# Performance work log

Hardware: AMD Instinct MI355X
Metric: run time of the kernel (lower is better)

Reference implementation:

```python
import jax, jax.numpy as jnp
import numpy as np

D_MODEL = 1024
N_HEADS = 16
D_HEAD = D_MODEL // N_HEADS
D_FF = 4096
EPS = 1e-5


def _layernorm(x, g, b):
    mu = jnp.mean(x, axis=-1, keepdims=True)
    var = jnp.mean(jnp.square(x - mu), axis=-1, keepdims=True)
    return (x - mu) * jax.lax.rsqrt(var + EPS) * g + b


def setup_inputs() -> dict:
    key = jax.random.key(0)
    ks = jax.random.split(key, 16)
    B, S, D = 2, 2048, D_MODEL

    def xavier(k, shape):
        fan_in, fan_out = shape[0], shape[1]
        lim = float(np.sqrt(6.0 / (fan_in + fan_out)))
        return jax.random.uniform(k, shape, jnp.float32, -lim, lim)

    return {
        "x": jax.random.normal(ks[0], (B, S, D), jnp.float32),
        "ln1_g": jnp.ones((D,), jnp.float32),
        "ln1_b": jnp.zeros((D,), jnp.float32),
        "wq": xavier(ks[1], (D, D)), "bq": jnp.zeros((D,), jnp.float32),
        "wk": xavier(ks[2], (D, D)), "bk": jnp.zeros((D,), jnp.float32),
        "wv": xavier(ks[3], (D, D)), "bv": jnp.zeros((D,), jnp.float32),
        "wo": xavier(ks[4], (D, D)), "bo": jnp.zeros((D,), jnp.float32),
        "wf": xavier(ks[5], (D, N_HEADS)), "bf": jnp.zeros((N_HEADS,), jnp.float32),
        "ln2_g": jnp.ones((D,), jnp.float32),
        "ln2_b": jnp.zeros((D,), jnp.float32),
        "w1": xavier(ks[6], (D, D_FF)), "b1": jnp.zeros((D_FF,), jnp.float32),
        "w2": xavier(ks[7], (D_FF, D)), "b2": jnp.zeros((D,), jnp.float32),
    }


def reference(x, ln1_g, ln1_b, wq, bq, wk, bk, wv, bv, wo, bo, wf, bf,
              ln2_g, ln2_b, w1, b1, w2, b2):
    B, S, D = x.shape
    H, Dh = N_HEADS, D_HEAD

    # --- pre-norm forgetting attention ---
    h = _layernorm(x, ln1_g, ln1_b)
    q = (h @ wq + bq).reshape(B, S, H, Dh)
    k = (h @ wk + bk).reshape(B, S, H, Dh)
    v = (h @ wv + bv).reshape(B, S, H, Dh)

    # per-head scalar forget gate f_t in (0,1); cumulative log-decay c_t
    logf = jax.nn.log_sigmoid(h @ wf + bf)           # (B, S, H)
    c = jnp.cumsum(logf, axis=1)                     # (B, S, H)

    scale = 1.0 / jnp.sqrt(jnp.asarray(Dh, x.dtype))
    logits = jnp.einsum("bihd,bjhd->bhij", q, k) * scale
    # decay bias D_ij = c_i - c_j (sum of log forget gates in (j, i])
    decay = c.transpose(0, 2, 1)                     # (B, H, S)
    logits = logits + decay[:, :, :, None] - decay[:, :, None, :]

    causal = jnp.tril(jnp.ones((S, S), bool))
    logits = jnp.where(causal[None, None], logits, -jnp.inf)

    attn = jax.nn.softmax(logits, axis=-1)           # (B, H, S, S)
    ctx = jnp.einsum("bhij,bjhd->bihd", attn, v).reshape(B, S, D)
    attn_out = ctx @ wo + bo

    x = x + attn_out                                 # dropout = identity (eval)

    # --- pre-norm GELU MLP ---
    h2 = _layernorm(x, ln2_g, ln2_b)
    ff = jax.nn.gelu(h2 @ w1 + b1, approximate=False) @ w2 + b2
    return x + ff
```

## Files before the change

kernel.cpp:

```cpp
#include <hip/hip_runtime.h>
#include <hip/hip_bf16.h>
#include <math.h>

typedef unsigned short u16;
typedef unsigned int u32;
typedef __bf16 bf16x8 __attribute__((ext_vector_type(8)));
typedef float f32x4 __attribute__((ext_vector_type(4)));
typedef u32 u32x4 __attribute__((ext_vector_type(4)));

__device__ __forceinline__ u16 f2bf(float f) {
  __hip_bfloat16 h = __float2bfloat16(f);
  return *reinterpret_cast<u16*>(&h);
}
__device__ __forceinline__ float bf2f(u16 u) {
  return __uint_as_float(((u32)u) << 16);
}

#define GLL(gp, lp)                                                     \
  __builtin_amdgcn_global_load_lds(                                     \
      (const __attribute__((address_space(1))) void*)(gp),              \
      (__attribute__((address_space(3))) void*)(lp), 16, 0, 0)

__global__ __launch_bounds__(256) void transpose_cast(
    const float* __restrict__ in, u16* __restrict__ out, int R, int C) {
  __shared__ float tile[32][33];
  int c0 = blockIdx.x * 32, r0 = blockIdx.y * 32;
  int tx = threadIdx.x & 31, ty = threadIdx.x >> 5;
  for (int i = ty; i < 32; i += 8) {
    int r = r0 + i, c = c0 + tx;
    if (r < R && c < C) tile[i][tx] = in[(size_t)r * C + c];
  }
  __syncthreads();
  for (int i = ty; i < 32; i += 8) {
    int c = c0 + i, r = r0 + tx;
    if (c < C && r < R) out[(size_t)c * R + r] = f2bf(tile[tx][i]);
  }
}

__global__ __launch_bounds__(256) void transpose_cast3(
    const float* __restrict__ in0, const float* __restrict__ in1,
    const float* __restrict__ in2, u16* __restrict__ out) {
  __shared__ float tile[32][33];
  const float* in = (blockIdx.z == 0) ? in0 : (blockIdx.z == 1) ? in1 : in2;
  u16* o = out + (size_t)blockIdx.z * 1024 * 1024;
  int c0 = blockIdx.x * 32, r0 = blockIdx.y * 32;
  int tx = threadIdx.x & 31, ty = threadIdx.x >> 5;
  for (int i = ty; i < 32; i += 8)
    tile[i][tx] = in[(size_t)(r0 + i) * 1024 + c0 + tx];
  __syncthreads();
  for (int i = ty; i < 32; i += 8)
    o[(size_t)(c0 + i) * 1024 + r0 + tx] = f2bf(tile[tx][i]);
}

__global__ __launch_bounds__(256) void pack3(
    const float* __restrict__ a, const float* __restrict__ b,
    const float* __restrict__ c, float* __restrict__ o, u32* __restrict__ ctr) {
  int t = blockIdx.x * 256 + threadIdx.x;
  if (t == 0) *ctr = 0u;
  if (t < 1024) o[t] = a[t];
  else if (t < 2048) o[t] = b[t - 1024];
  else if (t < 3072) o[t] = c[t - 2048];
}

__global__ __launch_bounds__(256) void ln_kernel(
    const float* x, const float* __restrict__ g,
    const float* __restrict__ bb, u16* __restrict__ out,
    float* xadd, const float* addb) {
  __shared__ float red[8];
  const int row = blockIdx.x;
  const float* xr = x + (size_t)row * 1024;
  f32x4 v = *(const f32x4*)(xr + threadIdx.x * 4);
  float s = v[0] + v[1] + v[2] + v[3];
  #pragma unroll
  for (int off = 32; off > 0; off >>= 1) s += __shfl_xor(s, off, 64);
  if ((threadIdx.x & 63) == 0) red[threadIdx.x >> 6] = s;
  __syncthreads();
  float mu = (red[0] + red[1] + red[2] + red[3]) * (1.0f / 1024.0f);
  f32x4 d;
  d[0] = v[0] - mu; d[1] = v[1] - mu; d[2] = v[2] - mu; d[3] = v[3] - mu;
  float sq = d[0]*d[0] + d[1]*d[1] + d[2]*d[2] + d[3]*d[3];
  #pragma unroll
  for (int off = 32; off > 0; off >>= 1) sq += __shfl_xor(sq, off, 64);
  if ((threadIdx.x & 63) == 0) red[4 + (threadIdx.x >> 6)] = sq;
  __syncthreads();
  float var = (red[4] + red[5] + red[6] + red[7]) * (1.0f / 1024.0f);
  float rstd = rsqrtf(var + 1e-5f);
  int cb = threadIdx.x * 4;
  #pragma unroll
  for (int e = 0; e < 4; ++e)
    out[(size_t)row * 1024 + cb + e] = f2bf(d[e] * rstd * g[cb + e] + bb[cb + e]);
  if (xadd) {
    f32x4 w;
    #pragma unroll
    for (int e = 0; e < 4; ++e) w[e] = v[e] + addb[cb + e];
    *(f32x4*)(xadd + (size_t)row * 1024 + cb) = w;
  }
}

__global__ __launch_bounds__(256) void gemm_bt(
    const u16* __restrict__ A, const u16* __restrict__ Bt,
    const float* __restrict__ bias, const float* __restrict__ res,
    void* __restrict__ outp, int M, int N, int K, int mode) {
  __shared__ u16 As[4 * 128 * 32];
  __shared__ u16 Bs[4 * 128 * 32];
  const int tid = threadIdx.x;
  const int m0 = blockIdx.y * 128, n0 = blockIdx.x * 128;
  const int wave = tid >> 6, lane = tid & 63;
  const int wm = (wave >> 1) * 64, wn = (wave & 1) * 64;
  const int lr = lane & 15, quad = lane >> 4;
  const int g0 = wave * 2;
  const int srow0 = g0 * 16 + (lane >> 2);
  const int scol = (lane & 3) * 8;
  const u16* Ag0 = A + (size_t)(m0 + srow0) * K + scol;
  const u16* Ag1 = A + (size_t)(m0 + srow0 + 16) * K + scol;
  const u16* Bg0 = Bt + (size_t)(n0 + srow0) * K + scol;
  const u16* Bg1 = Bt + (size_t)(n0 + srow0 + 16) * K + scol;
  const int ao0 = g0 * 512, ao1 = (g0 + 1) * 512;

  f32x4 acc[4][4] = {};

  GLL(Ag0, As + ao0); GLL(Ag1, As + ao1);
  GLL(Bg0, Bs + ao0); GLL(Bg1, Bs + ao1);
  if (K > 32) {
    GLL(Ag0 + 32, As + 4096 + ao0); GLL(Ag1 + 32, As + 4096 + ao1);
    GLL(Bg0 + 32, Bs + 4096 + ao0); GLL(Bg1 + 32, Bs + 4096 + ao1);
  }

  for (int k0 = 0; k0 < K; k0 += 32) {
    const int cb = ((k0 >> 5) & 3) * 4096;
    if (k0 + 64 < K) {
      const int pb = (((k0 >> 5) + 2) & 3) * 4096;
      GLL(Ag0 + k0 + 64, As + pb + ao0);
      GLL(Ag1 + k0 + 64, As + pb + ao1);
      GLL(Bg0 + k0 + 64, Bs + pb + ao0);
      GLL(Bg1 + k0 + 64, Bs + pb + ao1);
      asm volatile("s_waitcnt vmcnt(8)" ::: "memory");
    } else if (k0 + 32 < K) {
      asm volatile("s_waitcnt vmcnt(4)" ::: "memory");
    } else {
      asm volatile("s_waitcnt vmcnt(0)" ::: "memory");
    }
    __builtin_amdgcn_s_barrier();
    __builtin_amdgcn_sched_barrier(0);
    bf16x8 af[4], bfr[4];
    #pragma unroll
    for (int t = 0; t < 4; ++t) {
      af[t]  = *(const bf16x8*)&As[cb + (wm + t * 16 + lr) * 32 + quad * 8];
      bfr[t] = *(const bf16x8*)&Bs[cb + (wn + t * 16 + lr) * 32 + quad * 8];
    }
    #pragma unroll
    for (int mt = 0; mt < 4; ++mt)
      #pragma unroll
      for (int nt = 0; nt < 4; ++nt)
        acc[mt][nt] = __builtin_amdgcn_mfma_f32_16x16x32_bf16(
            af[mt], bfr[nt], acc[mt][nt], 0, 0, 0);
  }

  #pragma unroll
  for (int mt = 0; mt < 4; ++mt) {
    #pragma unroll
    for (int nt = 0; nt < 4; ++nt) {
      const int col = n0 + wn + nt * 16 + lr;
      const float bvv = bias[col];
      #pragma unroll
      for (int rr = 0; rr < 4; ++rr) {
        const int row = m0 + wm + mt * 16 + quad * 4 + rr;
        const size_t idx = (size_t)row * N + col;
        float v = acc[mt][nt][rr] + bvv;
        if (mode == 0) {
          ((float*)outp)[idx] = v;
        } else if (mode == 1) {
          ((float*)outp)[idx] = v + res[idx];
        } else if (mode == 2) {
          float gl = 0.5f * v * (1.0f + erff(v * 0.70710678118654752f));
          ((u16*)outp)[idx] = f2bf(gl);
        } else {
          ((u16*)outp)[idx] = f2bf(v);
        }
      }
    }
  }
}

__global__ __launch_bounds__(256) void gemm_bt_sk(
    const u16* __restrict__ A, const u16* __restrict__ Bt,
    float* __restrict__ outp, int M, int N, int Ktot, int Kslice) {
  __shared__ u16 As[4 * 128 * 32];
  __shared__ u16 Bs[4 * 128 * 32];
  const int tid = threadIdx.x;
  const int m0 = blockIdx.y * 128, n0 = blockIdx.x * 128;
  const int kbeg = blockIdx.z * Kslice, kend = kbeg + Kslice;
  const int wave = tid >> 6, lane = tid & 63;
  const int wm = (wave >> 1) * 64, wn = (wave & 1) * 64;
  const int lr = lane & 15, quad = lane >> 4;
  const int g0 = wave * 2;
  const int srow0 = g0 * 16 + (lane >> 2);
  const int scol = (lane & 3) * 8;
  const u16* Ag0 = A + (size_t)(m0 + srow0) * Ktot + scol;
  const u16* Ag1 = A + (size_t)(m0 + srow0 + 16) * Ktot + scol;
  const u16* Bg0 = Bt + (size_t)(n0 + srow0) * Ktot + scol;
  const u16* Bg1 = Bt + (size_t)(n0 + srow0 + 16) * Ktot + scol;
  const int ao0 = g0 * 512, ao1 = (g0 + 1) * 512;

  f32x4 acc[4][4] = {};

  GLL(Ag0 + kbeg, As + ao0); GLL(Ag1 + kbeg, As + ao1);
  GLL(Bg0 + kbeg, Bs + ao0); GLL(Bg1 + kbeg, Bs + ao1);
  if (kbeg + 32 < kend) {
    GLL(Ag0 + kbeg + 32, As + 4096 + ao0); GLL(Ag1 + kbeg + 32, As + 4096 + ao1);
    GLL(Bg0 + kbeg + 32, Bs + 4096 + ao0); GLL(Bg1 + kbeg + 32, Bs + 4096 + ao1);
  }

  for (int k0 = kbeg; k0 < kend; k0 += 32) {
    const int st = (k0 - kbeg) >> 5;
    const int cb = (st & 3) * 4096;
    if (k0 + 64 < kend) {
      const int pb = ((st + 2) & 3) * 4096;
      GLL(Ag0 + k0 + 64, As + pb + ao0);
      GLL(Ag1 + k0 + 64, As + pb + ao1);
      GLL(Bg0 + k0 + 64, Bs + pb + ao0);
      GLL(Bg1 + k0 + 64, Bs + pb + ao1);
      asm volatile("s_waitcnt vmcnt(8)" ::: "memory");
    } else if (k0 + 32 < kend) {
      asm volatile("s_waitcnt vmcnt(4)" ::: "memory");
    } else {
      asm volatile("s_waitcnt vmcnt(0)" ::: "memory");
    }
    __builtin_amdgcn_s_barrier();
    __builtin_amdgcn_sched_barrier(0);
    bf16x8 af[4], bfr[4];
    #pragma unroll
    for (int t = 0; t < 4; ++t) {
      af[t]  = *(const bf16x8*)&As[cb + (wm + t * 16 + lr) * 32 + quad * 8];
      bfr[t] = *(const bf16x8*)&Bs[cb + (wn + t * 16 + lr) * 32 + quad * 8];
    }
    #pragma unroll
    for (int mt = 0; mt < 4; ++mt)
      #pragma unroll
      for (int nt = 0; nt < 4; ++nt)
        acc[mt][nt] = __builtin_amdgcn_mfma_f32_16x16x32_bf16(
            af[mt], bfr[nt], acc[mt][nt], 0, 0, 0);
  }

  #pragma unroll
  for (int mt = 0; mt < 4; ++mt) {
    #pragma unroll
    for (int nt = 0; nt < 4; ++nt) {
      const int col = n0 + wn + nt * 16 + lr;
      #pragma unroll
      for (int rr = 0; rr < 4; ++rr) {
        const int row = m0 + wm + mt * 16 + quad * 4 + rr;
        __hip_atomic_fetch_add(&outp[(size_t)row * N + col], acc[mt][nt][rr],
                               __ATOMIC_RELAXED, __HIP_MEMORY_SCOPE_AGENT);
      }
    }
  }
}

__global__ __launch_bounds__(256) void gemm_n64(
    const u16* __restrict__ A, const u16* __restrict__ Bt,
    const float* __restrict__ bias, const float* __restrict__ res,
    void* __restrict__ outp, int M, int N, int K, int mode) {
  __shared__ u16 As[4 * 128 * 32];
  __shared__ u16 Bs[4 * 64 * 32];
  const int tid = threadIdx.x;
  const int m0 = blockIdx.y * 128, n0 = blockIdx.x * 64;
  const int wave = tid >> 6, lane = tid & 63;
  const int wm = (wave >> 1) * 64, wn = (wave & 1) * 32;
  const int lr = lane & 15, quad = lane >> 4;
  const int g0 = wave * 2;
  const int srow = lane >> 2;
  const int scol = (lane & 3) * 8;
  const u16* Ag0 = A + (size_t)(m0 + g0 * 16 + srow) * K + scol;
  const u16* Ag1 = A + (size_t)(m0 + g0 * 16 + 16 + srow) * K + scol;
  const u16* Bg  = Bt + (size_t)(n0 + wave * 16 + srow) * K + scol;
  const int ao0 = g0 * 512, ao1 = (g0 + 1) * 512, bo = wave * 512;

  f32x4 acc[4][2] = {};

  GLL(Ag0, As + ao0); GLL(Ag1, As + ao1); GLL(Bg, Bs + bo);
  if (K > 32) {
    GLL(Ag0 + 32, As + 4096 + ao0); GLL(Ag1 + 32, As + 4096 + ao1);
    GLL(Bg + 32, Bs + 2048 + bo);
  }

  for (int k0 = 0; k0 < K; k0 += 32) {
    const int st = k0 >> 5;
    const int cba = (st & 3) * 4096, cbb = (st & 3) * 2048;
    if (k0 + 64 < K) {
      const int pba = ((st + 2) & 3) * 4096, pbb = ((st + 2) & 3) * 2048;
      GLL(Ag0 + k0 + 64, As + pba + ao0);
      GLL(Ag1 + k0 + 64, As + pba + ao1);
      GLL(Bg + k0 + 64, Bs + pbb + bo);
      asm volatile("s_waitcnt vmcnt(6)" ::: "memory");
    } else if (k0 + 32 < K) {
      asm volatile("s_waitcnt vmcnt(3)" ::: "memory");
    } else {
      asm volatile("s_waitcnt vmcnt(0)" ::: "memory");
    }
    __builtin_amdgcn_s_barrier();
    __builtin_amdgcn_sched_barrier(0);
    bf16x8 af[4], bfr[2];
    #pragma unroll
    for (int t = 0; t < 4; ++t)
      af[t] = *(const bf16x8*)&As[cba + (wm + t * 16 + lr) * 32 + quad * 8];
    #pragma unroll
    for (int t = 0; t < 2; ++t)
      bfr[t] = *(const bf16x8*)&Bs[cbb + (wn + t * 16 + lr) * 32 + quad * 8];
    #pragma unroll
    for (int mt = 0; mt < 4; ++mt)
      #pragma unroll
      for (int nt = 0; nt < 2; ++nt)
        acc[mt][nt] = __builtin_amdgcn_mfma_f32_16x16x32_bf16(
            af[mt], bfr[nt], acc[mt][nt], 0, 0, 0);
  }

  #pragma unroll
  for (int mt = 0; mt < 4; ++mt) {
    #pragma unroll
    for (int nt = 0; nt < 2; ++nt) {
      const int col = n0 + wn + nt * 16 + lr;
      const float bvv = bias[col];
      #pragma unroll
      for (int rr = 0; rr < 4; ++rr) {
        const int row = m0 + wm + mt * 16 + quad * 4 + rr;
        const size_t idx = (size_t)row * N + col;
        float v = acc[mt][nt][rr] + bvv;
        if (mode == 0) {
          ((float*)outp)[idx] = v;
        } else if (mode == 1) {
          ((float*)outp)[idx] = v + res[idx];
        } else if (mode == 2) {
          float gl = 0.5f * v * (1.0f + erff(v * 0.70710678118654752f));
          ((u16*)outp)[idx] = f2bf(gl);
        } else {
          ((u16*)outp)[idx] = f2bf(v);
        }
      }
    }
  }
}

__global__ __launch_bounds__(64) void logf_kernel(
    const u16* __restrict__ h, const u16* __restrict__ wfT,
    const float* __restrict__ bfv, float* __restrict__ c) {
  const int row = blockIdx.x;
  const int lane = threadIdx.x;
  float acc[16];
  #pragma unroll
  for (int n = 0; n < 16; ++n) acc[n] = 0.f;
  for (int t = 0; t < 16; ++t) {
    int kidx = t * 64 + lane;
    float hv = bf2f(h[(size_t)row * 1024 + kidx]);
    #pragma unroll
    for (int n = 0; n < 16; ++n)
      acc[n] += hv * bf2f(wfT[n * 1024 + kidx]);
  }
  float z = 0.f;
  #pragma unroll
  for (int n = 0; n < 16; ++n) {
    float r = acc[n];
    #pragma unroll
    for (int off = 1; off < 64; off <<= 1) r += __shfl_xor(r, off, 64);
    if (lane == n) z = r;
  }
  if (lane < 16) {
    z += bfv[lane];
    float lf = (z >= 0.f) ? -log1pf(expf(-z)) : (z - log1pf(expf(z)));
    c[(size_t)row * 16 + lane] = lf;
  }
}

__global__ __launch_bounds__(64) void cumsum_kernel(float* __restrict__ c, int S) {
  const int b = blockIdx.x >> 4, h = blockIdx.x & 15;
  const int lane = threadIdx.x;
  float carry = 0.f;
  for (int s0 = 0; s0 < S; s0 += 64) {
    float v = c[(size_t)(b * S + s0 + lane) * 16 + h];
    #pragma unroll
    for (int off = 1; off < 64; off <<= 1) {
      float t = __shfl_up(v, off, 64);
      if (lane >= off) v += t;
    }
    v += carry;
    c[(size_t)(b * S + s0 + lane) * 16 + h] = v;
    carry = __shfl(v, 63, 64);
  }
}

__global__ __launch_bounds__(256) void vtrans(
    const u16* __restrict__ qkvb, u16* __restrict__ vtg) {
  __shared__ u16 t[32][33];
  const int bh = blockIdx.z, b = bh >> 4, h = bh & 15;
  const int s0 = blockIdx.x * 32, d0 = blockIdx.y * 32;
  const int tx = threadIdx.x & 31, ty = threadIdx.x >> 5;
  for (int i = ty; i < 32; i += 8)
    t[i][tx] = qkvb[(size_t)(b * 2048 + s0 + i) * 3072 + 2048 + h * 64 + d0 + tx];
  __syncthreads();
  for (int i = ty; i < 32; i += 8)
    vtg[(size_t)(bh * 64 + d0 + i) * 2048 + s0 + tx] = t[tx][i];
}

__global__ __launch_bounds__(64) void qk_norms(
    const u16* __restrict__ qkvb, float* __restrict__ qkmax) {
  const int tile = blockIdx.x, bh = blockIdx.y, z = blockIdx.z;
  const int b = bh >> 4, h = bh & 15;
  const int tok = tile * 64 + (int)threadIdx.x;
  const u16* p = qkvb + (size_t)(b * 2048 + tok) * 3072 + z * 1024 + h * 64;
  float s = 0.f;
  #pragma unroll
  for (int i = 0; i < 4; ++i) {
    u32x4 w = *(const u32x4*)(p + i * 16);
    u32x4 w2 = *(const u32x4*)(p + i * 16 + 8);
    #pragma unroll
    for (int e = 0; e < 4; ++e) {
      float lo = __uint_as_float(w[e] << 16);
      float hi = __uint_as_float(w[e] & 0xffff0000u);
      float lo2 = __uint_as_float(w2[e] << 16);
      float hi2 = __uint_as_float(w2[e] & 0xffff0000u);
      s += lo * lo + hi * hi + lo2 * lo2 + hi2 * hi2;
    }
  }
  s = sqrtf(s);
  #pragma unroll
  for (int off = 1; off < 64; off <<= 1) s = fmaxf(s, __shfl_xor(s, off, 64));
  if (threadIdx.x == 0) qkmax[z * 1024 + bh * 32 + tile] = s;
}

#define FS 72
#define NITEMS 1024
#define L2E 1.4426950408889634f

__global__ __launch_bounds__(256) void fattn(
    const u16* __restrict__ qkvb, const u16* __restrict__ vtg,
    const float* __restrict__ c, const float* __restrict__ qkmax,
    u16* __restrict__ ctx, u32* __restrict__ ctr) {
  __shared__ u16 Qs[64 * FS];
  __shared__ u16 Ks[64 * FS];
  __shared__ u16 Vt[64 * FS];
  __shared__ u16 Ps[64 * FS];
  __shared__ float cjs[64];
  __shared__ float wmn[4];
  __shared__ u32 sh_item;
  const int S = 2048;
  const int tid = threadIdx.x, wave = tid >> 6, lane = tid & 63;
  const int lr = lane & 15, quad = lane >> 4;
  const int w16 = wave * 16;
  const int sr = tid >> 2, scc = (tid & 3) * 16;

  for (;;) {
    if (tid == 0) sh_item = atomicAdd(ctr, 1u);
    __syncthreads();
    const u32 item = sh_item;
    if (item >= NITEMS) return;
    const int qt = 31 - (int)(item >> 5);
    const int bh = (int)(item & 31), b = bh >> 4, h = bh & 15;
    const int i0 = qt * 64;

    {
      const u16* src = qkvb + (size_t)(b * S + i0 + sr) * 3072 + h * 64 + scc;
      *(u32x4*)&Qs[sr * FS + scc] = *(const u32x4*)src;
      *(u32x4*)&Qs[sr * FS + scc + 8] = *(const u32x4*)(src + 8);
    }
    u32x4 kr0, kr1, vr0, vr1;
    float cjr = 0.f;
    {
      const u16* ks = qkvb + (size_t)(b * S + i0 + sr) * 3072 + 1024 + h * 64 + scc;
      kr0 = *(const u32x4*)ks;
      kr1 = *(const u32x4*)(ks + 8);
      const u16* vs = vtg + (size_t)(bh * 64 + sr) * 2048 + i0 + scc;
      vr0 = *(const u32x4*)vs;
      vr1 = *(const u32x4*)(vs + 8);
      if (tid < 64) cjr = c[(size_t)(b * S + i0 + tid) * 16 + h];
    }
    float bscale;
    {
      float qm = qkmax[bh * 32 + qt];
      float km = 0.f;
      for (int t = 0; t <= qt; ++t) km = fmaxf(km, qkmax[1024 + bh * 32 + t]);
      bscale = qm * km * (0.125f * L2E);
    }
    float m_[4], l_[4], alpha[4];
    f32x4 o_[4];
    #pragma unroll
    for (int r = 0; r < 4; ++r) {
      m_[r] = -INFINITY;
      l_[r] = 0.f;
    }
    #pragma unroll
    for (int dt = 0; dt < 4; ++dt) o_[dt] = (f32x4){0.f, 0.f, 0.f, 0.f};

    __syncthreads();
    const bf16x8 aq0 = *(const bf16x8*)&Qs[(w16 + lr) * FS + quad * 8];
    const bf16x8 aq1 = *(const bf16x8*)&Qs[(w16 + lr) * FS + 32 + quad * 8];

    for (int jt = qt; jt >= 0; --jt) {
      const int j0 = jt * 64;
      *(u32x4*)&Ks[sr * FS + scc] = kr0;
      *(u32x4*)&Ks[sr * FS + scc + 8] = kr1;
      *(u32x4*)&Vt[sr * FS + scc] = vr0;
      *(u32x4*)&Vt[sr * FS + scc + 8] = vr1;
      if (tid < 64) cjs[tid] = cjr * L2E;
      if (jt > 0) {
        const int j1 = j0 - 64;
        const u16* ks = qkvb + (size_t)(b * S + j1 + sr) * 3072 + 1024 + h * 64 + scc;
        kr0 = *(const u32x4*)ks;
        kr1 = *(const u32x4*)(ks + 8);
        const u16* vs = vtg + (size_t)(bh * 64 + sr) * 2048 + j1 + scc;
        vr0 = *(const u32x4*)vs;
        vr1 = *(const u32x4*)(vs + 8);
        if (tid < 64) cjr = c[(size_t)(b * S + j1 + tid) * 16 + h];
      }
      __syncthreads();

      f32x4 sc[4];
      #pragma unroll
      for (int nt = 0; nt < 4; ++nt) {
        bf16x8 bk0 = *(const bf16x8*)&Ks[(nt * 16 + lr) * FS + quad * 8];
        bf16x8 bk1 = *(const bf16x8*)&Ks[(nt * 16 + lr) * FS + 32 + quad * 8];
        f32x4 z = {0.f, 0.f, 0.f, 0.f};
        z = __builtin_amdgcn_mfma_f32_16x16x32_bf16(aq0, bk0, z, 0, 0, 0);
        z = __builtin_amdgcn_mfma_f32_16x16x32_bf16(aq1, bk1, z, 0, 0, 0);
        sc[nt] = z;
      }
      const bool diag = (jt == qt);
      #pragma unroll
      for (int r = 0; r < 4; ++r) {
        const int i = i0 + w16 + quad * 4 + r;
        float lg[4], mrow = -INFINITY;
        #pragma unroll
        for (int nt = 0; nt < 4; ++nt) {
          const int j = j0 + nt * 16 + lr;
          float v = sc[nt][r] * (0.125f * L2E) - cjs[nt * 16 + lr];
          if (diag && (j > i)) v = -INFINITY;
          lg[nt] = v;
          mrow = fmaxf(mrow, v);
        }
        #pragma unroll
        for (int off = 1; off < 16; off <<= 1)
          mrow = fmaxf(mrow, __shfl_xor(mrow, off, 64));
        const float mn = fmaxf(m_[r], mrow);
        alpha[r] = __builtin_exp2f(m_[r] - mn);
        m_[r] = mn;
        float rs = 0.f;
        #pragma unroll
        for (int nt = 0; nt < 4; ++nt) {
          const float p = __builtin_exp2f(lg[nt] - mn);
          Ps[(w16 + quad * 4 + r) * FS + nt * 16 + lr] = f2bf(p);
          rs += p;
        }
        l_[r] = l_[r] * alpha[r] + rs;
      }
      asm volatile("s_waitcnt lgkmcnt(0)" ::: "memory");
      #pragma unroll
      for (int dt = 0; dt < 4; ++dt)
        #pragma unroll
        for (int r = 0; r < 4; ++r) o_[dt][r] *= alpha[r];
      bf16x8 ap0 = *(const bf16x8*)&Ps[(w16 + lr) * FS + quad * 8];
      bf16x8 ap1 = *(const bf16x8*)&Ps[(w16 + lr) * FS + 32 + quad * 8];
      #pragma unroll
      for (int dt = 0; dt < 4; ++dt) {
        bf16x8 bv0 = *(const bf16x8*)&Vt[(dt * 16 + lr) * FS + quad * 8];
        bf16x8 bv1 = *(const bf16x8*)&Vt[(dt * 16 + lr) * FS + 32 + quad * 8];
        o_[dt] = __builtin_amdgcn_mfma_f32_16x16x32_bf16(ap0, bv0, o_[dt], 0, 0, 0);
        o_[dt] = __builtin_amdgcn_mfma_f32_16x16x32_bf16(ap1, bv1, o_[dt], 0, 0, 0);
      }
      {
        float wmin = fminf(fminf(m_[0], m_[1]), fminf(m_[2], m_[3]));
        wmin = fminf(wmin, __shfl_xor(wmin, 16, 64));
        wmin = fminf(wmin, __shfl_xor(wmin, 32, 64));
        if (lane == 0) wmn[wave] = wmin;
      }
      __syncthreads();
      if (jt > 0) {
        const float bmin = fminf(fminf(wmn[0], wmn[1]), fminf(wmn[2], wmn[3]));
        const float cend = c[(size_t)(b * S + j0 - 1) * 16 + h];
        if (bscale - cend * L2E < bmin - 40.f) break;
      }
    }
    #pragma unroll
    for (int r = 0; r < 4; ++r) {
      float lt = l_[r];
      #pragma unroll
      for (int off = 1; off < 16; off <<= 1) lt += __shfl_xor(lt, off, 64);
      const float inv = 1.0f / lt;
      const size_t base = (size_t)(b * S + i0 + w16 + quad * 4 + r) * 1024 + h * 64;
      #pragma unroll
      for (int dt = 0; dt < 4; ++dt)
        ctx[base + dt * 16 + lr] = f2bf(o_[dt][r] * inv);
    }
  }
}

extern "C" void kernel_launch(void* const* d_in, const int* in_sizes, int n_in,
                              void* d_out, int out_size, void* d_ws, size_t ws_size,
                              hipStream_t stream) {
  const float* x    = (const float*)d_in[0];
  const float* ln1g = (const float*)d_in[1];
  const float* ln1b = (const float*)d_in[2];
  const float* wq   = (const float*)d_in[3];
  const float* bq   = (const float*)d_in[4];
  const float* wk   = (const float*)d_in[5];
  const float* bk   = (const float*)d_in[6];
  const float* wv   = (const float*)d_in[7];
  const float* bv   = (const float*)d_in[8];
  const float* wo   = (const float*)d_in[9];
  const float* bo   = (const float*)d_in[10];
  const float* wf   = (const float*)d_in[11];
  const float* bfv  = (const float*)d_in[12];
  const float* ln2g = (const float*)d_in[13];
  const float* ln2b = (const float*)d_in[14];
  const float* w1   = (const float*)d_in[15];
  const float* b1   = (const float*)d_in[16];
  const float* w2   = (const float*)d_in[17];
  const float* b2   = (const float*)d_in[18];
  float* out = (float*)d_out;

  char* ws = (char*)d_ws;
  const size_t MB = 1024 * 1024;
  u16*   wqkvT = (u16*)(ws + 0 * MB);
  u16*   woT   = (u16*)(ws + 6 * MB);
  u16*   w1T   = (u16*)(ws + 8 * MB);
  u16*   w2T   = (u16*)(ws + 16 * MB);
  u16*   wfT   = (u16*)(ws + 24 * MB);
  float* bqkv  = (float*)(ws + 24 * MB + 65536);
  u32*   fctr  = (u32*)(ws + 24 * MB + 131072);
  u16*   hbuf  = (u16*)(ws + 25 * MB);
  u16*   ctx   = (u16*)(ws + 33 * MB);
  u16*   qkvb  = (u16*)(ws + 41 * MB);
  u16*   vtg   = (u16*)(ws + 65 * MB);
  float* cb    = (float*)(ws + 73 * MB);
  float* qkmax = (float*)(ws + 73 * MB + 262144);
  u16*   act1  = (u16*)(ws + 74 * MB);

  dim3 blk(256);
  transpose_cast3<<<dim3(32, 32, 3), blk, 0, stream>>>(wq, wk, wv, wqkvT);
  transpose_cast<<<dim3(32, 32), blk, 0, stream>>>(wo, woT, 1024, 1024);
  transpose_cast<<<dim3(128, 32), blk, 0, stream>>>(w1, w1T, 1024, 4096);
  transpose_cast<<<dim3(32, 128), blk, 0, stream>>>(w2, w2T, 4096, 1024);
  transpose_cast<<<dim3(1, 32), blk, 0, stream>>>(wf, wfT, 1024, 16);
  pack3<<<12, blk, 0, stream>>>(bq, bk, bv, bqkv, fctr);
  ln_kernel<<<4096, blk, 0, stream>>>(x, ln1g, ln1b, hbuf, nullptr, nullptr);
  gemm_bt<<<dim3(24, 32), blk, 0, stream>>>(hbuf, wqkvT, bqkv, nullptr, qkvb,
                                            4096, 3072, 1024, 3);
  logf_kernel<<<4096, dim3(64), 0, stream>>>(hbuf, wfT, bfv, cb);
  cumsum_kernel<<<32, dim3(64), 0, stream>>>(cb, 2048);
  vtrans<<<dim3(64, 2, 32), blk, 0, stream>>>(qkvb, vtg);
  qk_norms<<<dim3(32, 32, 2), dim3(64), 0, stream>>>(qkvb, qkmax);
  fattn<<<dim3(1024), blk, 0, stream>>>(qkvb, vtg, cb, qkmax, ctx, fctr);
  gemm_n64<<<dim3(16, 32), blk, 0, stream>>>(ctx, woT, bo, x, out,
                                             4096, 1024, 1024, 1);
  ln_kernel<<<4096, blk, 0, stream>>>(out, ln2g, ln2b, hbuf, out, b2);
  gemm_bt<<<dim3(32, 32), blk, 0, stream>>>(hbuf, w1T, b1, nullptr, act1,
                                            4096, 4096, 1024, 2);
  gemm_bt_sk<<<dim3(8, 32, 2), blk, 0, stream>>>(act1, w2T, out,
                                                 4096, 1024, 4096, 2048);
}
```

Measured before the change: 470.9 us.

## Use three-stage LDS ring with extra barrier and MFMA priority in GEMMs

Shrinks the shared-memory ring in the three GEMM kernels from four stages to three, with a rotating stage index replacing the modulo-4 arithmetic. A second barrier after the fragment reads makes the smaller ring safe, since a stage can now be overwritten two iterations later. The MFMA block is also wrapped in s_setprio(1)/s_setprio(0). The goal is to cut LDS use so more blocks fit per CU and to favor math issue, at the cost of one extra barrier per K step.

```diff
diff --git a/kernel.cpp b/kernel.cpp
--- a/kernel.cpp
+++ b/kernel.cpp
@@ -101,8 +101,8 @@
     const u16* __restrict__ A, const u16* __restrict__ Bt,
     const float* __restrict__ bias, const float* __restrict__ res,
     void* __restrict__ outp, int M, int N, int K, int mode) {
-  __shared__ u16 As[4 * 128 * 32];
-  __shared__ u16 Bs[4 * 128 * 32];
+  __shared__ u16 As[3 * 128 * 32];
+  __shared__ u16 Bs[3 * 128 * 32];
   const int tid = threadIdx.x;
   const int m0 = blockIdx.y * 128, n0 = blockIdx.x * 128;
   const int wave = tid >> 6, lane = tid & 63;
@@ -126,10 +126,12 @@
     GLL(Bg0 + 32, Bs + 4096 + ao0); GLL(Bg1 + 32, Bs + 4096 + ao1);
   }
 
+  int cur = 0;
   for (int k0 = 0; k0 < K; k0 += 32) {
-    const int cb = ((k0 >> 5) & 3) * 4096;
+    const int cb = cur * 4096;
     if (k0 + 64 < K) {
-      const int pb = (((k0 >> 5) + 2) & 3) * 4096;
+      int ns = cur + 2; if (ns >= 3) ns -= 3;
+      const int pb = ns * 4096;
       GLL(Ag0 + k0 + 64, As + pb + ao0);
       GLL(Ag1 + k0 + 64, As + pb + ao1);
       GLL(Bg0 + k0 + 64, Bs + pb + ao0);
@@ -148,12 +150,18 @@
       af[t]  = *(const bf16x8*)&As[cb + (wm + t * 16 + lr) * 32 + quad * 8];
       bfr[t] = *(const bf16x8*)&Bs[cb + (wn + t * 16 + lr) * 32 + quad * 8];
     }
+    asm volatile("s_waitcnt lgkmcnt(0)" ::: "memory");
+    __builtin_amdgcn_sched_barrier(0);
+    __builtin_amdgcn_s_barrier();
+    __builtin_amdgcn_s_setprio(1);
     #pragma unroll
     for (int mt = 0; mt < 4; ++mt)
       #pragma unroll
       for (int nt = 0; nt < 4; ++nt)
         acc[mt][nt] = __builtin_amdgcn_mfma_f32_16x16x32_bf16(
             af[mt], bfr[nt], acc[mt][nt], 0, 0, 0);
+    __builtin_amdgcn_s_setprio(0);
+    cur += 1; if (cur >= 3) cur = 0;
   }
 
   #pragma unroll
@@ -185,8 +193,8 @@
 __global__ __launch_bounds__(256) void gemm_bt_sk(
     const u16* __restrict__ A, const u16* __restrict__ Bt,
     float* __restrict__ outp, int M, int N, int Ktot, int Kslice) {
-  __shared__ u16 As[4 * 128 * 32];
-  __shared__ u16 Bs[4 * 128 * 32];
+  __shared__ u16 As[3 * 128 * 32];
+  __shared__ u16 Bs[3 * 128 * 32];
   const int tid = threadIdx.x;
   const int m0 = blockIdx.y * 128, n0 = blockIdx.x * 128;
   const int kbeg = blockIdx.z * Kslice, kend = kbeg + Kslice;
@@ -211,11 +219,12 @@
     GLL(Bg0 + kbeg + 32, Bs + 4096 + ao0); GLL(Bg1 + kbeg + 32, Bs + 4096 + ao1);
   }
 
+  int cur = 0;
   for (int k0 = kbeg; k0 < kend; k0 += 32) {
-    const int st = (k0 - kbeg) >> 5;
-    const int cb = (st & 3) * 4096;
+    const int cb = cur * 4096;
     if (k0 + 64 < kend) {
-      const int pb = ((st + 2) & 3) * 4096;
+      int ns = cur + 2; if (ns >= 3) ns -= 3;
+      const int pb = ns * 4096;
       GLL(Ag0 + k0 + 64, As + pb + ao0);
       GLL(Ag1 + k0 + 64, As + pb + ao1);
       GLL(Bg0 + k0 + 64, Bs + pb + ao0);
@@ -234,12 +243,18 @@
       af[t]  = *(const bf16x8*)&As[cb + (wm + t * 16 + lr) * 32 + quad * 8];
       bfr[t] = *(const bf16x8*)&Bs[cb + (wn + t * 16 + lr) * 32 + quad * 8];
     }
+    asm volatile("s_waitcnt lgkmcnt(0)" ::: "memory");
+    __builtin_amdgcn_sched_barrier(0);
+    __builtin_amdgcn_s_barrier();
+    __builtin_amdgcn_s_setprio(1);
     #pragma unroll
     for (int mt = 0; mt < 4; ++mt)
       #pragma unroll
       for (int nt = 0; nt < 4; ++nt)
         acc[mt][nt] = __builtin_amdgcn_mfma_f32_16x16x32_bf16(
             af[mt], bfr[nt], acc[mt][nt], 0, 0, 0);
+    __builtin_amdgcn_s_setprio(0);
+    cur += 1; if (cur >= 3) cur = 0;
   }
 
   #pragma unroll
@@ -261,8 +276,8 @@
     const u16* __restrict__ A, const u16* __restrict__ Bt,
     const float* __restrict__ bias, const float* __restrict__ res,
     void* __restrict__ outp, int M, int N, int K, int mode) {
-  __shared__ u16 As[4 * 128 * 32];
-  __shared__ u16 Bs[4 * 64 * 32];
+  __shared__ u16 As[3 * 128 * 32];
+  __shared__ u16 Bs[3 * 64 * 32];
   const int tid = threadIdx.x;
   const int m0 = blockIdx.y * 128, n0 = blockIdx.x * 64;
   const int wave = tid >> 6, lane = tid & 63;
@@ -284,14 +299,14 @@
     GLL(Bg + 32, Bs + 2048 + bo);
   }
 
+  int cur = 0;
   for (int k0 = 0; k0 < K; k0 += 32) {
-    const int st = k0 >> 5;
-    const int cba = (st & 3) * 4096, cbb = (st & 3) * 2048;
+    const int cba = cur * 4096, cbb = cur * 2048;
     if (k0 + 64 < K) {
-      const int pba = ((st + 2) & 3) * 4096, pbb = ((st + 2) & 3) * 2048;
-      GLL(Ag0 + k0 + 64, As + pba + ao0);
-      GLL(Ag1 + k0 + 64, As + pba + ao1);
-      GLL(Bg + k0 + 64, Bs + pbb + bo);
+      int ns = cur + 2; if (ns >= 3) ns -= 3;
+      GLL(Ag0 + k0 + 64, As + ns * 4096 + ao0);
+      GLL(Ag1 + k0 + 64, As + ns * 4096 + ao1);
+      GLL(Bg + k0 + 64, Bs + ns * 2048 + bo);
       asm volatile("s_waitcnt vmcnt(6)" ::: "memory");
     } else if (k0 + 32 < K) {
       asm volatile("s_waitcnt vmcnt(3)" ::: "memory");
@@ -307,12 +322,18 @@
     #pragma unroll
     for (int t = 0; t < 2; ++t)
       bfr[t] = *(const bf16x8*)&Bs[cbb + (wn + t * 16 + lr) * 32 + quad * 8];
+    asm volatile("s_waitcnt lgkmcnt(0)" ::: "memory");
+    __builtin_amdgcn_sched_barrier(0);
+    __builtin_amdgcn_s_barrier();
+    __builtin_amdgcn_s_setprio(1);
     #pragma unroll
     for (int mt = 0; mt < 4; ++mt)
       #pragma unroll
       for (int nt = 0; nt < 2; ++nt)
         acc[mt][nt] = __builtin_amdgcn_mfma_f32_16x16x32_bf16(
             af[mt], bfr[nt], acc[mt][nt], 0, 0, 0);
+    __builtin_amdgcn_s_setprio(0);
+    cur += 1; if (cur >= 3) cur = 0;
   }
 
   #pragma unroll
```

New measurement: 465.6 us. Within noise of the previous version (-1.1%).
